# Performance work log

Hardware: AMD Instinct MI355X
Metric: run time of the kernel (lower is better)

## Reference

```python
import jax, jax.numpy as jnp
import numpy as np

N_NODES = 12288
N_FEATURES = 256
KEY_DIM = 128
N_GRAPHS = 192


def setup_inputs() -> dict:
    key = jax.random.key(0)
    k1, k2, k3, k4, k5 = jax.random.split(key, 5)
    node_out = jax.random.normal(k1, (N_NODES, N_FEATURES), dtype=jnp.float32)
    batch = jnp.sort(jax.random.randint(k2, (N_NODES,), 0, N_GRAPHS, dtype=jnp.int64))
    # xavier_uniform: limit = sqrt(6 / (fan_in + fan_out))
    lim_qk = float(np.sqrt(6.0 / (N_FEATURES + KEY_DIM)))
    lim_v = float(np.sqrt(6.0 / (N_FEATURES + N_FEATURES)))
    query_weight = jax.random.uniform(k3, (N_FEATURES, KEY_DIM), jnp.float32, -lim_qk, lim_qk)
    key_weight = jax.random.uniform(k4, (N_FEATURES, KEY_DIM), jnp.float32, -lim_qk, lim_qk)
    value_weight = jax.random.uniform(k5, (N_FEATURES, N_FEATURES), jnp.float32, -lim_v, lim_v)
    return {
        "node_out": node_out,
        "batch": batch,
        "query_weight": query_weight,
        "key_weight": key_weight,
        "value_weight": value_weight,
    }


def reference(node_out, batch, query_weight, key_weight, value_weight):
    n_features = node_out.shape[1]
    Q = node_out @ query_weight            # [N, K]
    K = node_out @ key_weight              # [N, K]
    V = node_out @ value_weight            # [N, F]
    # NOTE: original scales by sqrt(n_features), not sqrt(key_dim)
    scores = (Q @ K.T) / jnp.sqrt(jnp.asarray(n_features, dtype=Q.dtype))  # [N, N]
    mask = batch[:, None] == batch[None, :]  # block-diagonal per-graph mask
    scores = jnp.where(mask, scores, -jnp.inf)
    attn = jax.nn.softmax(scores, axis=-1)   # every row has >=1 valid entry
    context = attn @ V                        # [N, F]
    return jax.ops.segment_sum(context, batch, num_segments=N_GRAPHS)  # [G, F]
```

## Files before the change

kernel.cpp:

```cpp
#include <hip/hip_runtime.h>
#include <hip/hip_bf16.h>

#define N_NODES  12288
#define N_FEAT   256
#define KDIM     128
#define N_GRAPHS 192
#define NMAX     112
#define KSTRIDE_U 68

#define MT   32
#define XS_STRIDE_U 36
#define WT_STRIDE_U 36

#define WS_STARTS 0
#define WS_WBUF   1024
#define WS_U      (WS_WBUF + N_NODES * 4)
#define WS_QB     (WS_U + N_GRAPHS * N_FEAT * 4)
#define WS_KB     (WS_QB + N_NODES * 64 * 4)
#define WS_WT     (WS_KB + N_NODES * 64 * 4)

typedef __bf16 bf16x8 __attribute__((ext_vector_type(8)));
typedef float  f32x4  __attribute__((ext_vector_type(4)));

__device__ __forceinline__ unsigned bf16_rne(float f) {
  unsigned u = __float_as_uint(f);
  return (u + 0x7FFFu + ((u >> 16) & 1u)) >> 16;
}
__device__ __forceinline__ unsigned pack_bf16(float lo, float hi) {
  return bf16_rne(lo) | (bf16_rne(hi) << 16);
}
__device__ __forceinline__ float bf_lo(unsigned u) { return __uint_as_float(u << 16); }
__device__ __forceinline__ float bf_hi(unsigned u) { return __uint_as_float(u & 0xFFFF0000u); }

__global__ __launch_bounds__(256) void seg_starts_k(const int* __restrict__ batch,
                                                    int* __restrict__ starts) {
  int g = threadIdx.x;
  if (g > N_GRAPHS) return;
  int lo = 0, hi = N_NODES;
  while (lo < hi) {
    int mid = (lo + hi) >> 1;
    if (batch[mid] < g) lo = mid + 1; else hi = mid;
  }
  starts[g] = lo;
}

__global__ __launch_bounds__(64) void wt_prep_k(const float* __restrict__ Wq,
                                                const float* __restrict__ Wk,
                                                unsigned* __restrict__ Wt) {
  const int n = blockIdx.x;
  const int t = threadIdx.x;
  const float* src = (n < KDIM) ? (Wq + n) : (Wk + (n - KDIM));
  float f0 = src[(4 * t + 0) * KDIM];
  float f1 = src[(4 * t + 1) * KDIM];
  float f2 = src[(4 * t + 2) * KDIM];
  float f3 = src[(4 * t + 3) * KDIM];
  Wt[n * 128 + 2 * t]     = pack_bf16(f0, f1);
  Wt[n * 128 + 2 * t + 1] = pack_bf16(f2, f3);
}

__global__ __launch_bounds__(256) void qk_proj_k(const float* __restrict__ X,
                                                 const unsigned* __restrict__ Wt,
                                                 unsigned* __restrict__ Qb,
                                                 unsigned* __restrict__ Kb) {
  __shared__ unsigned Xs_u[MT * XS_STRIDE_U];
  __shared__ unsigned Ws_u[256 * WT_STRIDE_U];

  const int tid  = threadIdx.x;
  const int lane = tid & 63;
  const int wv   = tid >> 6;
  const int r0   = blockIdx.x * MT;
  const int l15  = lane & 15;
  const int quad = lane >> 4;

  f32x4 acc[2][4];
#pragma unroll
  for (int mi = 0; mi < 2; mi++)
#pragma unroll
    for (int ni = 0; ni < 4; ni++) acc[mi][ni] = (f32x4){0.f, 0.f, 0.f, 0.f};

  for (int c = 0; c < 4; c++) {
    const int k0 = c * 64;
    if (c) __syncthreads();

    {
      const int row = tid >> 3, c8 = tid & 7;
      const float* xp = &X[(size_t)(r0 + row) * N_FEAT + k0 + c8 * 8];
      float4 a = *(const float4*)xp;
      float4 b = *(const float4*)(xp + 4);
      unsigned p0 = pack_bf16(a.x, a.y), p1 = pack_bf16(a.z, a.w);
      unsigned p2 = pack_bf16(b.x, b.y), p3 = pack_bf16(b.z, b.w);
      *(uint4*)&Xs_u[row * XS_STRIDE_U + c8 * 4] = make_uint4(p0, p1, p2, p3);
    }
#pragma unroll
    for (int it = 0; it < 8; it++) {
      const int i = tid + it * 256;
      const int n = i >> 3, c8 = i & 7;
      uint4 w = *(const uint4*)&Wt[n * 128 + k0 / 2 + c8 * 4];
      *(uint4*)&Ws_u[n * WT_STRIDE_U + c8 * 4] = w;
    }
    __syncthreads();

#pragma unroll
    for (int ks = 0; ks < 2; ks++) {
      const int ko = ks * 16 + quad * 4;
      bf16x8 a[2], b[4];
#pragma unroll
      for (int mi = 0; mi < 2; mi++)
        a[mi] = *(const bf16x8*)&Xs_u[(mi * 16 + l15) * XS_STRIDE_U + ko];
#pragma unroll
      for (int ni = 0; ni < 4; ni++)
        b[ni] = *(const bf16x8*)&Ws_u[(wv * 64 + ni * 16 + l15) * WT_STRIDE_U + ko];
#pragma unroll
      for (int mi = 0; mi < 2; mi++)
#pragma unroll
        for (int ni = 0; ni < 4; ni++)
          acc[mi][ni] = __builtin_amdgcn_mfma_f32_16x16x32_bf16(a[mi], b[ni], acc[mi][ni], 0, 0, 0);
    }
  }

  unsigned* dst = (wv < 2) ? Qb : Kb;
  const float scale = (wv < 2) ? 0.0625f : 1.0f;
  const int colbase = (wv & 1) * 64;
#pragma unroll
  for (int mi = 0; mi < 2; mi++)
#pragma unroll
    for (int ni = 0; ni < 4; ni++) {
      const int col = colbase + ni * 16 + l15;
#pragma unroll
      for (int e = 0; e < 4; e++) {
        const int row = r0 + mi * 16 + quad * 4 + e;
        unsigned b = bf16_rne(acc[mi][ni][e] * scale);
        unsigned partner = __shfl_xor((int)b, 1);
        if ((lane & 1) == 0)
          dst[row * 64 + (col >> 1)] = b | (partner << 16);
      }
    }
}

__global__ __launch_bounds__(256) void attn_w_k(const int* __restrict__ starts,
                                                const unsigned* __restrict__ Qb,
                                                const unsigned* __restrict__ Kb,
                                                float* __restrict__ wbuf) {
  __shared__ unsigned Ks_u[NMAX * KSTRIDE_U];
  __shared__ float    w_lds[4][NMAX];

  const int tid  = threadIdx.x;
  const int lane = tid & 63;
  const int wv   = tid >> 6;
  const int l15  = lane & 15;
  const int quad = lane >> 4;
  const int g    = blockIdx.x >> 1;
  const int qi   = blockIdx.x & 1;

  const int i0 = starts[g];
  const int n  = starts[g + 1] - i0;
  const float BIG = 1e30f;
  const bool fast = (n <= NMAX);
  if (!fast && qi != 0) return;

  float wl[7];
#pragma unroll
  for (int f = 0; f < 7; f++) wl[f] = 0.f;

  if (fast) {
    for (int idx = tid; idx < n * 16; idx += 256) {
      int j = idx >> 4, c = idx & 15;
      *(uint4*)&Ks_u[j * KSTRIDE_U + 4 * c] = *(const uint4*)&Kb[(size_t)(i0 + j) * 64 + 4 * c];
    }
    __syncthreads();

    const int ns = (n + 15) >> 4;
    const int s  = qi + 2 * wv;

    if (s < ns && n > 0) {
      const int arow = min(s * 16 + l15, n - 1);
      const unsigned* qrow = &Qb[(size_t)(i0 + arow) * 64];
      bf16x8 au[4];
#pragma unroll
      for (int ks = 0; ks < 4; ks++)
        au[ks] = *(const bf16x8*)&qrow[ks * 16 + quad * 4];

      f32x4 acc[7];
#pragma unroll
      for (int f = 0; f < 7; f++) acc[f] = (f32x4){0.f, 0.f, 0.f, 0.f};
#pragma unroll
      for (int f = 0; f < 7; f++) {
#pragma unroll
        for (int ks = 0; ks < 4; ks++) {
          bf16x8 bu = *(const bf16x8*)&Ks_u[(f * 16 + l15) * KSTRIDE_U + ks * 16 + quad * 4];
          acc[f] = __builtin_amdgcn_mfma_f32_16x16x32_bf16(au[ks], bu, acc[f], 0, 0, 0);
        }
      }

      const bool colv = true;
#pragma unroll
      for (int f = 0; f < 7; f++) {
        if (f * 16 + l15 >= n) {
          acc[f][0] = -BIG; acc[f][1] = -BIG; acc[f][2] = -BIG; acc[f][3] = -BIG;
        }
      }
      (void)colv;

#pragma unroll
      for (int e = 0; e < 4; e++) {
        float m = -BIG;
#pragma unroll
        for (int f = 0; f < 7; f++) m = fmaxf(m, acc[f][e]);
        m = fmaxf(m, __shfl_xor(m, 1));
        m = fmaxf(m, __shfl_xor(m, 2));
        m = fmaxf(m, __shfl_xor(m, 4));
        m = fmaxf(m, __shfl_xor(m, 8));
        float p[7], l = 0.f;
#pragma unroll
        for (int f = 0; f < 7; f++) { p[f] = __expf(acc[f][e] - m); l += p[f]; }
        l += __shfl_xor(l, 1);
        l += __shfl_xor(l, 2);
        l += __shfl_xor(l, 4);
        l += __shfl_xor(l, 8);
        const int row = s * 16 + quad * 4 + e;
        float inv = (row < n) ? (1.f / l) : 0.f;
#pragma unroll
        for (int f = 0; f < 7; f++) wl[f] = fmaf(p[f], inv, wl[f]);
      }
    }

#pragma unroll
    for (int f = 0; f < 7; f++) {
      wl[f] += __shfl_xor(wl[f], 16);
      wl[f] += __shfl_xor(wl[f], 32);
    }
    if (lane < 16) {
#pragma unroll
      for (int f = 0; f < 7; f++) w_lds[wv][f * 16 + lane] = wl[f];
    }
    __syncthreads();

    if (tid < n && tid < NMAX) {
      float t = w_lds[0][tid] + w_lds[1][tid] + w_lds[2][tid] + w_lds[3][tid];
      atomicAdd(&wbuf[i0 + tid], t);
    }
  } else {
    for (int lr = wv; lr < n; lr += 4) {
      const uint4* qp4 = (const uint4*)&Qb[(size_t)(i0 + lr) * 64];
      float m_run = -BIG, l_run = 0.f;
      for (int jb = 0; jb < n; jb += 64) {
        int j = jb + lane;
        int jc = min(j, n - 1);
        const uint4* kp4 = (const uint4*)&Kb[(size_t)(i0 + jc) * 64];
        float s = 0.f;
        for (int c = 0; c < 16; c++) {
          uint4 Q1 = qp4[c];
          uint4 K1 = kp4[c];
          s = fmaf(bf_lo(Q1.x), bf_lo(K1.x), s); s = fmaf(bf_hi(Q1.x), bf_hi(K1.x), s);
          s = fmaf(bf_lo(Q1.y), bf_lo(K1.y), s); s = fmaf(bf_hi(Q1.y), bf_hi(K1.y), s);
          s = fmaf(bf_lo(Q1.z), bf_lo(K1.z), s); s = fmaf(bf_hi(Q1.z), bf_hi(K1.z), s);
          s = fmaf(bf_lo(Q1.w), bf_lo(K1.w), s); s = fmaf(bf_hi(Q1.w), bf_hi(K1.w), s);
        }
        if (j >= n) s = -BIG;
        float mc = s;
        for (int off = 32; off; off >>= 1) mc = fmaxf(mc, __shfl_xor(mc, off));
        float m_new = fmaxf(m_run, mc);
        float lc = __expf(s - m_new);
        for (int off = 32; off; off >>= 1) lc += __shfl_xor(lc, off);
        l_run = l_run * __expf(m_run - m_new) + lc;
        m_run = m_new;
      }
      float inv = 1.f / l_run;
      for (int jb = 0; jb < n; jb += 64) {
        int j = jb + lane;
        int jc = min(j, n - 1);
        const uint4* kp4 = (const uint4*)&Kb[(size_t)(i0 + jc) * 64];
        float s = 0.f;
        for (int c = 0; c < 16; c++) {
          uint4 Q1 = qp4[c];
          uint4 K1 = kp4[c];
          s = fmaf(bf_lo(Q1.x), bf_lo(K1.x), s); s = fmaf(bf_hi(Q1.x), bf_hi(K1.x), s);
          s = fmaf(bf_lo(Q1.y), bf_lo(K1.y), s); s = fmaf(bf_hi(Q1.y), bf_hi(K1.y), s);
          s = fmaf(bf_lo(Q1.z), bf_lo(K1.z), s); s = fmaf(bf_hi(Q1.z), bf_hi(K1.z), s);
          s = fmaf(bf_lo(Q1.w), bf_lo(K1.w), s); s = fmaf(bf_hi(Q1.w), bf_hi(K1.w), s);
        }
        if (j < n) atomicAdd(&wbuf[i0 + j], __expf(s - m_run) * inv);
      }
    }
  }
}

__global__ __launch_bounds__(512) void vout_u_k(const float* __restrict__ X,
                                                const int* __restrict__ starts,
                                                const float* __restrict__ wbuf,
                                                float* __restrict__ U) {
  __shared__ float part[4][128];
  const int g   = blockIdx.x >> 1;
  const int fh  = blockIdx.x & 1;
  const int tid = threadIdx.x;
  const int fl  = tid & 127;
  const int f   = fh * 128 + fl;
  const int jp  = tid >> 7;

  const int i0 = starts[g];
  const int n  = starts[g + 1] - i0;

  float ua = 0.f, ub = 0.f;
  int j = jp;
  for (; j + 4 < n; j += 8) {
    ua = fmaf(wbuf[i0 + j],     X[(size_t)(i0 + j) * N_FEAT + f], ua);
    ub = fmaf(wbuf[i0 + j + 4], X[(size_t)(i0 + j + 4) * N_FEAT + f], ub);
  }
  for (; j < n; j += 4)
    ua = fmaf(wbuf[i0 + j], X[(size_t)(i0 + j) * N_FEAT + f], ua);
  part[jp][fl] = ua + ub;
  __syncthreads();
  if (jp == 0)
    U[g * N_FEAT + f] = (part[0][fl] + part[1][fl]) + (part[2][fl] + part[3][fl]);
}

__global__ __launch_bounds__(512) void vout_o_k(const float* __restrict__ U,
                                                const float* __restrict__ Wv,
                                                float* __restrict__ out) {
  __shared__ float Us[256];
  __shared__ float part[4][128];
  const int g   = blockIdx.x >> 1;
  const int fh  = blockIdx.x & 1;
  const int tid = threadIdx.x;
  const int fl  = tid & 127;
  const int f   = fh * 128 + fl;
  const int kq  = tid >> 7;

  if (tid < 256) Us[tid] = U[g * N_FEAT + tid];
  __syncthreads();

  const int k0 = kq * 64;
  const float* wp = Wv + (size_t)k0 * N_FEAT + f;
  const float* us = &Us[k0];
  float a0 = 0.f, a1 = 0.f, a2 = 0.f, a3 = 0.f;
#pragma unroll 4
  for (int k = 0; k < 64; k += 4) {
    a0 = fmaf(us[k],     wp[(size_t)k * N_FEAT], a0);
    a1 = fmaf(us[k + 1], wp[(size_t)(k + 1) * N_FEAT], a1);
    a2 = fmaf(us[k + 2], wp[(size_t)(k + 2) * N_FEAT], a2);
    a3 = fmaf(us[k + 3], wp[(size_t)(k + 3) * N_FEAT], a3);
  }
  part[kq][fl] = (a0 + a1) + (a2 + a3);
  __syncthreads();
  if (kq == 0)
    out[g * N_FEAT + f] = (part[0][fl] + part[1][fl]) + (part[2][fl] + part[3][fl]);
}

extern "C" void kernel_launch(void* const* d_in, const int* in_sizes, int n_in,
                              void* d_out, int out_size, void* d_ws, size_t ws_size,
                              hipStream_t stream) {
  const float* X     = (const float*)d_in[0];
  const int*   batch = (const int*)d_in[1];
  const float* Wq    = (const float*)d_in[2];
  const float* Wk    = (const float*)d_in[3];
  const float* Wv    = (const float*)d_in[4];
  float* out = (float*)d_out;

  char* ws = (char*)d_ws;
  int*      starts = (int*)(ws + WS_STARTS);
  float*    wbuf   = (float*)(ws + WS_WBUF);
  float*    U      = (float*)(ws + WS_U);
  unsigned* Qb     = (unsigned*)(ws + WS_QB);
  unsigned* Kb     = (unsigned*)(ws + WS_KB);
  unsigned* Wt     = (unsigned*)(ws + WS_WT);

  hipMemsetAsync(ws + WS_WBUF, 0, (N_NODES + N_GRAPHS * N_FEAT) * 4, stream);
  seg_starts_k<<<1, 256, 0, stream>>>(batch, starts);
  wt_prep_k<<<256, 64, 0, stream>>>(Wq, Wk, Wt);
  qk_proj_k<<<N_NODES / MT, 256, 0, stream>>>(X, Wt, Qb, Kb);
  attn_w_k<<<N_GRAPHS * 2, 256, 0, stream>>>(starts, Qb, Kb, wbuf);
  vout_u_k<<<N_GRAPHS * 2, 512, 0, stream>>>(X, starts, wbuf, U);
  vout_o_k<<<N_GRAPHS * 2, 512, 0, stream>>>(U, Wv, out);
}
```

Baseline: 99.55 us.

## Fuse attention, pooling and value projection into one per-graph kernel

Merges the segment-start search into the weight-prep kernel and fuses attention weighting, weighted pooling and the Wv projection into a single per-graph kernel with 512 threads. Attention weights stay in LDS instead of going through a global buffer with atomics. The memset and two launches are dropped. The Q/K projection now uses 16-row tiles and reads Wt directly from global memory instead of staging it in LDS. This cuts launch overhead and global round-trips, but uses only 192 blocks for the fused kernel, so occupancy and parallelism drop.

```diff
diff --git a/kernel.cpp b/kernel.cpp
--- a/kernel.cpp
+++ b/kernel.cpp
@@ -7,15 +7,11 @@
 #define N_GRAPHS 192
 #define NMAX     112
 #define KSTRIDE_U 68
-
-#define MT   32
-#define XS_STRIDE_U 36
-#define WT_STRIDE_U 36
+#define XS_STRIDE_U 132
 
 #define WS_STARTS 0
 #define WS_WBUF   1024
-#define WS_U      (WS_WBUF + N_NODES * 4)
-#define WS_QB     (WS_U + N_GRAPHS * N_FEAT * 4)
+#define WS_QB     (WS_WBUF + N_NODES * 4)
 #define WS_KB     (WS_QB + N_NODES * 64 * 4)
 #define WS_WT     (WS_KB + N_NODES * 64 * 4)
 
@@ -32,21 +28,11 @@
 __device__ __forceinline__ float bf_lo(unsigned u) { return __uint_as_float(u << 16); }
 __device__ __forceinline__ float bf_hi(unsigned u) { return __uint_as_float(u & 0xFFFF0000u); }
 
-__global__ __launch_bounds__(256) void seg_starts_k(const int* __restrict__ batch,
-                                                    int* __restrict__ starts) {
-  int g = threadIdx.x;
-  if (g > N_GRAPHS) return;
-  int lo = 0, hi = N_NODES;
-  while (lo < hi) {
-    int mid = (lo + hi) >> 1;
-    if (batch[mid] < g) lo = mid + 1; else hi = mid;
-  }
-  starts[g] = lo;
-}
-
 __global__ __launch_bounds__(64) void wt_prep_k(const float* __restrict__ Wq,
                                                 const float* __restrict__ Wk,
-                                                unsigned* __restrict__ Wt) {
+                                                const int* __restrict__ batch,
+                                                unsigned* __restrict__ Wt,
+                                                int* __restrict__ starts) {
   const int n = blockIdx.x;
   const int t = threadIdx.x;
   const float* src = (n < KDIM) ? (Wq + n) : (Wk + (n - KDIM));
@@ -56,123 +42,116 @@
   float f3 = src[(4 * t + 3) * KDIM];
   Wt[n * 128 + 2 * t]     = pack_bf16(f0, f1);
   Wt[n * 128 + 2 * t + 1] = pack_bf16(f2, f3);
+
+  if (t == 0 && n <= N_GRAPHS) {
+    int lo = 0, hi = N_NODES;
+    while (lo < hi) {
+      int mid = (lo + hi) >> 1;
+      if (batch[mid] < n) lo = mid + 1; else hi = mid;
+    }
+    starts[n] = lo;
+  }
 }
 
 __global__ __launch_bounds__(256) void qk_proj_k(const float* __restrict__ X,
                                                  const unsigned* __restrict__ Wt,
                                                  unsigned* __restrict__ Qb,
                                                  unsigned* __restrict__ Kb) {
-  __shared__ unsigned Xs_u[MT * XS_STRIDE_U];
-  __shared__ unsigned Ws_u[256 * WT_STRIDE_U];
+  __shared__ unsigned Xs_u[16 * XS_STRIDE_U];
 
   const int tid  = threadIdx.x;
   const int lane = tid & 63;
   const int wv   = tid >> 6;
-  const int r0   = blockIdx.x * MT;
+  const int r0   = blockIdx.x * 16;
   const int l15  = lane & 15;
   const int quad = lane >> 4;
 
-  f32x4 acc[2][4];
-#pragma unroll
-  for (int mi = 0; mi < 2; mi++)
-#pragma unroll
-    for (int ni = 0; ni < 4; ni++) acc[mi][ni] = (f32x4){0.f, 0.f, 0.f, 0.f};
-
-  for (int c = 0; c < 4; c++) {
-    const int k0 = c * 64;
-    if (c) __syncthreads();
-
-    {
-      const int row = tid >> 3, c8 = tid & 7;
-      const float* xp = &X[(size_t)(r0 + row) * N_FEAT + k0 + c8 * 8];
-      float4 a = *(const float4*)xp;
-      float4 b = *(const float4*)(xp + 4);
-      unsigned p0 = pack_bf16(a.x, a.y), p1 = pack_bf16(a.z, a.w);
-      unsigned p2 = pack_bf16(b.x, b.y), p3 = pack_bf16(b.z, b.w);
-      *(uint4*)&Xs_u[row * XS_STRIDE_U + c8 * 4] = make_uint4(p0, p1, p2, p3);
-    }
-#pragma unroll
-    for (int it = 0; it < 8; it++) {
-      const int i = tid + it * 256;
-      const int n = i >> 3, c8 = i & 7;
-      uint4 w = *(const uint4*)&Wt[n * 128 + k0 / 2 + c8 * 4];
-      *(uint4*)&Ws_u[n * WT_STRIDE_U + c8 * 4] = w;
-    }
-    __syncthreads();
-
-#pragma unroll
-    for (int ks = 0; ks < 2; ks++) {
-      const int ko = ks * 16 + quad * 4;
-      bf16x8 a[2], b[4];
-#pragma unroll
-      for (int mi = 0; mi < 2; mi++)
-        a[mi] = *(const bf16x8*)&Xs_u[(mi * 16 + l15) * XS_STRIDE_U + ko];
-#pragma unroll
-      for (int ni = 0; ni < 4; ni++)
-        b[ni] = *(const bf16x8*)&Ws_u[(wv * 64 + ni * 16 + l15) * WT_STRIDE_U + ko];
-#pragma unroll
-      for (int mi = 0; mi < 2; mi++)
-#pragma unroll
-        for (int ni = 0; ni < 4; ni++)
-          acc[mi][ni] = __builtin_amdgcn_mfma_f32_16x16x32_bf16(a[mi], b[ni], acc[mi][ni], 0, 0, 0);
-    }
+  {
+    const int row = tid >> 4, seg = tid & 15;
+    const float* xp = &X[(size_t)(r0 + row) * N_FEAT + seg * 16];
+    float4 a = *(const float4*)xp;
+    float4 b = *(const float4*)(xp + 4);
+    float4 c = *(const float4*)(xp + 8);
+    float4 d = *(const float4*)(xp + 12);
+    unsigned* dst = &Xs_u[row * XS_STRIDE_U + seg * 8];
+    *(uint4*)dst       = make_uint4(pack_bf16(a.x, a.y), pack_bf16(a.z, a.w),
+                                    pack_bf16(b.x, b.y), pack_bf16(b.z, b.w));
+    *(uint4*)(dst + 4) = make_uint4(pack_bf16(c.x, c.y), pack_bf16(c.z, c.w),
+                                    pack_bf16(d.x, d.y), pack_bf16(d.z, d.w));
+  }
+  __syncthreads();
+
+  f32x4 acc[4];
+#pragma unroll
+  for (int ni = 0; ni < 4; ni++) acc[ni] = (f32x4){0.f, 0.f, 0.f, 0.f};
+
+#pragma unroll
+  for (int ks = 0; ks < 8; ks++) {
+    bf16x8 a = *(const bf16x8*)&Xs_u[l15 * XS_STRIDE_U + ks * 16 + quad * 4];
+    bf16x8 b[4];
+#pragma unroll
+    for (int ni = 0; ni < 4; ni++)
+      b[ni] = *(const bf16x8*)&Wt[(size_t)(wv * 64 + ni * 16 + l15) * 128 + ks * 16 + quad * 4];
+#pragma unroll
+    for (int ni = 0; ni < 4; ni++)
+      acc[ni] = __builtin_amdgcn_mfma_f32_16x16x32_bf16(a, b[ni], acc[ni], 0, 0, 0);
   }
 
   unsigned* dst = (wv < 2) ? Qb : Kb;
   const float scale = (wv < 2) ? 0.0625f : 1.0f;
   const int colbase = (wv & 1) * 64;
 #pragma unroll
-  for (int mi = 0; mi < 2; mi++)
-#pragma unroll
-    for (int ni = 0; ni < 4; ni++) {
-      const int col = colbase + ni * 16 + l15;
-#pragma unroll
-      for (int e = 0; e < 4; e++) {
-        const int row = r0 + mi * 16 + quad * 4 + e;
-        unsigned b = bf16_rne(acc[mi][ni][e] * scale);
-        unsigned partner = __shfl_xor((int)b, 1);
-        if ((lane & 1) == 0)
-          dst[row * 64 + (col >> 1)] = b | (partner << 16);
-      }
-    }
-}
-
-__global__ __launch_bounds__(256) void attn_w_k(const int* __restrict__ starts,
-                                                const unsigned* __restrict__ Qb,
-                                                const unsigned* __restrict__ Kb,
-                                                float* __restrict__ wbuf) {
+  for (int ni = 0; ni < 4; ni++) {
+    const int col = colbase + ni * 16 + l15;
+#pragma unroll
+    for (int e = 0; e < 4; e++) {
+      const int row = r0 + quad * 4 + e;
+      unsigned b = bf16_rne(acc[ni][e] * scale);
+      unsigned partner = __shfl_xor((int)b, 1);
+      if ((lane & 1) == 0)
+        dst[row * 64 + (col >> 1)] = b | (partner << 16);
+    }
+  }
+}
+
+__global__ __launch_bounds__(512) void attn_pool_k(const float* __restrict__ X,
+                                                   const int* __restrict__ starts,
+                                                   const unsigned* __restrict__ Qb,
+                                                   const unsigned* __restrict__ Kb,
+                                                   const float* __restrict__ Wv,
+                                                   float* __restrict__ out,
+                                                   float* __restrict__ wbuf) {
   __shared__ unsigned Ks_u[NMAX * KSTRIDE_U];
-  __shared__ float    w_lds[4][NMAX];
+  __shared__ float    w_lds[8][NMAX];
+  __shared__ float    red[2][256];
+  __shared__ float    Us[256];
 
   const int tid  = threadIdx.x;
   const int lane = tid & 63;
   const int wv   = tid >> 6;
   const int l15  = lane & 15;
   const int quad = lane >> 4;
-  const int g    = blockIdx.x >> 1;
-  const int qi   = blockIdx.x & 1;
+  const int g    = blockIdx.x;
 
   const int i0 = starts[g];
   const int n  = starts[g + 1] - i0;
   const float BIG = 1e30f;
   const bool fast = (n <= NMAX);
-  if (!fast && qi != 0) return;
-
-  float wl[7];
-#pragma unroll
-  for (int f = 0; f < 7; f++) wl[f] = 0.f;
 
   if (fast) {
-    for (int idx = tid; idx < n * 16; idx += 256) {
+    for (int idx = tid; idx < n * 16; idx += 512) {
       int j = idx >> 4, c = idx & 15;
       *(uint4*)&Ks_u[j * KSTRIDE_U + 4 * c] = *(const uint4*)&Kb[(size_t)(i0 + j) * 64 + 4 * c];
     }
     __syncthreads();
 
+    float wl[7];
+#pragma unroll
+    for (int f = 0; f < 7; f++) wl[f] = 0.f;
+
     const int ns = (n + 15) >> 4;
-    const int s  = qi + 2 * wv;
-
-    if (s < ns && n > 0) {
+    if (wv < ns) {
+      const int s = wv;
       const int arow = min(s * 16 + l15, n - 1);
       const unsigned* qrow = &Qb[(size_t)(i0 + arow) * 64];
       bf16x8 au[4];
@@ -191,15 +170,11 @@
           acc[f] = __builtin_amdgcn_mfma_f32_16x16x32_bf16(au[ks], bu, acc[f], 0, 0, 0);
         }
       }
-
-      const bool colv = true;
-#pragma unroll
-      for (int f = 0; f < 7; f++) {
+#pragma unroll
+      for (int f = 0; f < 7; f++)
         if (f * 16 + l15 >= n) {
           acc[f][0] = -BIG; acc[f][1] = -BIG; acc[f][2] = -BIG; acc[f][3] = -BIG;
         }
-      }
-      (void)colv;
 
 #pragma unroll
       for (int e = 0; e < 4; e++) {
@@ -235,12 +210,17 @@
     }
     __syncthreads();
 
-    if (tid < n && tid < NMAX) {
-      float t = w_lds[0][tid] + w_lds[1][tid] + w_lds[2][tid] + w_lds[3][tid];
-      atomicAdd(&wbuf[i0 + tid], t);
-    }
+    if (tid < NMAX) {
+      float t = 0.f;
+#pragma unroll
+      for (int k = 0; k < 8; k++) t += w_lds[k][tid];
+      w_lds[0][tid] = t;
+    }
+    __syncthreads();
   } else {
-    for (int lr = wv; lr < n; lr += 4) {
+    for (int idx = tid; idx < n; idx += 512) wbuf[i0 + idx] = 0.f;
+    __syncthreads();
+    for (int lr = wv; lr < n; lr += 8) {
       const uint4* qp4 = (const uint4*)&Qb[(size_t)(i0 + lr) * 64];
       float m_run = -BIG, l_run = 0.f;
       for (int jb = 0; jb < n; jb += 64) {
@@ -282,68 +262,47 @@
         if (j < n) atomicAdd(&wbuf[i0 + j], __expf(s - m_run) * inv);
       }
     }
-  }
-}
-
-__global__ __launch_bounds__(512) void vout_u_k(const float* __restrict__ X,
-                                                const int* __restrict__ starts,
-                                                const float* __restrict__ wbuf,
-                                                float* __restrict__ U) {
-  __shared__ float part[4][128];
-  const int g   = blockIdx.x >> 1;
-  const int fh  = blockIdx.x & 1;
-  const int tid = threadIdx.x;
-  const int fl  = tid & 127;
-  const int f   = fh * 128 + fl;
-  const int jp  = tid >> 7;
-
-  const int i0 = starts[g];
-  const int n  = starts[g + 1] - i0;
-
+    __threadfence();
+    __syncthreads();
+  }
+
+  const int f  = tid & 255;
+  const int jp = tid >> 8;
   float ua = 0.f, ub = 0.f;
-  int j = jp;
-  for (; j + 4 < n; j += 8) {
-    ua = fmaf(wbuf[i0 + j],     X[(size_t)(i0 + j) * N_FEAT + f], ua);
-    ub = fmaf(wbuf[i0 + j + 4], X[(size_t)(i0 + j + 4) * N_FEAT + f], ub);
-  }
-  for (; j < n; j += 4)
-    ua = fmaf(wbuf[i0 + j], X[(size_t)(i0 + j) * N_FEAT + f], ua);
-  part[jp][fl] = ua + ub;
-  __syncthreads();
-  if (jp == 0)
-    U[g * N_FEAT + f] = (part[0][fl] + part[1][fl]) + (part[2][fl] + part[3][fl]);
-}
-
-__global__ __launch_bounds__(512) void vout_o_k(const float* __restrict__ U,
-                                                const float* __restrict__ Wv,
-                                                float* __restrict__ out) {
-  __shared__ float Us[256];
-  __shared__ float part[4][128];
-  const int g   = blockIdx.x >> 1;
-  const int fh  = blockIdx.x & 1;
-  const int tid = threadIdx.x;
-  const int fl  = tid & 127;
-  const int f   = fh * 128 + fl;
-  const int kq  = tid >> 7;
-
-  if (tid < 256) Us[tid] = U[g * N_FEAT + tid];
-  __syncthreads();
-
-  const int k0 = kq * 64;
+  if (fast) {
+    int j = jp;
+    for (; j + 2 < n; j += 4) {
+      ua = fmaf(w_lds[0][j],     X[(size_t)(i0 + j) * N_FEAT + f], ua);
+      ub = fmaf(w_lds[0][j + 2], X[(size_t)(i0 + j + 2) * N_FEAT + f], ub);
+    }
+    for (; j < n; j += 2)
+      ua = fmaf(w_lds[0][j], X[(size_t)(i0 + j) * N_FEAT + f], ua);
+  } else {
+    for (int j = jp; j < n; j += 2) {
+      float wj = atomicAdd(&wbuf[i0 + j], 0.f);
+      ua = fmaf(wj, X[(size_t)(i0 + j) * N_FEAT + f], ua);
+    }
+  }
+  red[jp][f] = ua + ub;
+  __syncthreads();
+  if (jp == 0) Us[f] = red[0][f] + red[1][f];
+  __syncthreads();
+
+  const int k0 = jp * 128;
   const float* wp = Wv + (size_t)k0 * N_FEAT + f;
   const float* us = &Us[k0];
   float a0 = 0.f, a1 = 0.f, a2 = 0.f, a3 = 0.f;
-#pragma unroll 4
-  for (int k = 0; k < 64; k += 4) {
+#pragma unroll 8
+  for (int k = 0; k < 128; k += 4) {
     a0 = fmaf(us[k],     wp[(size_t)k * N_FEAT], a0);
     a1 = fmaf(us[k + 1], wp[(size_t)(k + 1) * N_FEAT], a1);
     a2 = fmaf(us[k + 2], wp[(size_t)(k + 2) * N_FEAT], a2);
     a3 = fmaf(us[k + 3], wp[(size_t)(k + 3) * N_FEAT], a3);
   }
-  part[kq][fl] = (a0 + a1) + (a2 + a3);
-  __syncthreads();
-  if (kq == 0)
-    out[g * N_FEAT + f] = (part[0][fl] + part[1][fl]) + (part[2][fl] + part[3][fl]);
+  __syncthreads();
+  red[jp][f] = (a0 + a1) + (a2 + a3);
+  __syncthreads();
+  if (jp == 0) out[g * N_FEAT + f] = red[0][f] + red[1][f];
 }
 
 extern "C" void kernel_launch(void* const* d_in, const int* in_sizes, int n_in,
@@ -359,16 +318,11 @@
   char* ws = (char*)d_ws;
   int*      starts = (int*)(ws + WS_STARTS);
   float*    wbuf   = (float*)(ws + WS_WBUF);
-  float*    U      = (float*)(ws + WS_U);
   unsigned* Qb     = (unsigned*)(ws + WS_QB);
   unsigned* Kb     = (unsigned*)(ws + WS_KB);
   unsigned* Wt     = (unsigned*)(ws + WS_WT);
 
-  hipMemsetAsync(ws + WS_WBUF, 0, (N_NODES + N_GRAPHS * N_FEAT) * 4, stream);
-  seg_starts_k<<<1, 256, 0, stream>>>(batch, starts);
-  wt_prep_k<<<256, 64, 0, stream>>>(Wq, Wk, Wt);
-  qk_proj_k<<<N_NODES / MT, 256, 0, stream>>>(X, Wt, Qb, Kb);
-  attn_w_k<<<N_GRAPHS * 2, 256, 0, stream>>>(starts, Qb, Kb, wbuf);
-  vout_u_k<<<N_GRAPHS * 2, 512, 0, stream>>>(X, starts, wbuf, U);
-  vout_o_k<<<N_GRAPHS * 2, 512, 0, stream>>>(U, Wv, out);
-}
+  wt_prep_k<<<256, 64, 0, stream>>>(Wq, Wk, batch, Wt, starts);
+  qk_proj_k<<<N_NODES / 16, 256, 0, stream>>>(X, Wt, Qb, Kb);
+  attn_pool_k<<<N_GRAPHS, 512, 0, stream>>>(X, starts, Qb, Kb, Wv, out, wbuf);
+}
```

New measurement: 98.17 us (median of 2 runs). Within noise of the previous version (-1.4%).
